# Kernel optimization log

Hardware: AMD Instinct MI355X
Metric: run time of the kernel (lower is better)

Reference implementation:

```python
import jax, jax.numpy as jnp
import numpy as np
from math import sqrt

EMBED = 1024
HEADS = 16

def setup_inputs() -> dict:
    key = jax.random.key(0)
    k1, k2, k3, k4, k5 = jax.random.split(key, 5)
    x = jax.random.normal(k1, (2, 2048, EMBED), dtype=jnp.float32)
    s = 1.0 / sqrt(EMBED)
    W_qkv = jax.random.normal(k2, (EMBED, 3 * EMBED), dtype=jnp.float32) * s
    b_qkv = jax.random.normal(k3, (3 * EMBED,), dtype=jnp.float32) * 0.01
    W_out = jax.random.normal(k4, (EMBED, EMBED), dtype=jnp.float32) * s
    b_out = jax.random.normal(k5, (EMBED,), dtype=jnp.float32) * 0.01
    return {"x": x, "W_qkv": W_qkv, "b_qkv": b_qkv, "W_out": W_out, "b_out": b_out}

def reference(x, W_qkv, b_qkv, W_out, b_out) -> jnp.ndarray:
    B, N, E = x.shape
    H = HEADS
    d = E // H
    qkv = x @ W_qkv + b_qkv                       # [B, N, 3E]
    q, k, v = jnp.split(qkv, 3, axis=2)
    # b n (h e) -> b n h e
    q = q.reshape(B, N, H, d)
    k = k.reshape(B, N, H, d)
    v = v.reshape(B, N, H, d)
    energy = jnp.einsum('bqhe,bkhe->bqhk', q, k)  # [B, N, H, N]
    # NOTE: original divides AFTER softmax, by sqrt(embed_size) (not head dim)
    attn = jax.nn.softmax(energy, axis=-1) / sqrt(E)
    out = jnp.einsum('bihv,bvhd->bihd', attn, v)  # [B, N, H, d]
    out = out.reshape(B, N, E)
    # dropout in eval mode -> identity
    return out @ W_out + b_out
```

## Files before the change

### kernel.cpp

```cpp
#include <hip/hip_runtime.h>
#include <hip/hip_bf16.h>

#define EMBED 1024
#define HEADS 16
#define HDIM 64
#define BATCH 2
#define SEQ 2048
#define ROWS (BATCH*SEQ)
#define QKV_N (3*EMBED)

typedef __attribute__((ext_vector_type(8))) short bf16x8;
typedef __attribute__((ext_vector_type(4))) float f32x4;
typedef __attribute__((ext_vector_type(16))) float f32x16;
typedef __hip_bfloat16 bf16;

__device__ inline f32x4 mfma16(bf16x8 a, bf16x8 b, f32x4 c) {
  return __builtin_amdgcn_mfma_f32_16x16x32_bf16(a, b, c, 0, 0, 0);
}
__device__ inline f32x16 mfma32(bf16x8 a, bf16x8 b, f32x16 c) {
  return __builtin_amdgcn_mfma_f32_32x32x16_bf16(a, b, c, 0, 0, 0);
}
__device__ inline unsigned pk2(float a, float b) {
  union { unsigned u; unsigned short s[2]; } r;
  union { bf16 h; unsigned short v; } ca, cb;
  ca.h = __float2bfloat16(a); cb.h = __float2bfloat16(b);
  r.s[0] = ca.v; r.s[1] = cb.v;
  return r.u;
}

__device__ inline void gload_lds16(const bf16* g, bf16* l) {
  __builtin_amdgcn_global_load_lds(
      (const __attribute__((address_space(1))) unsigned int*)g,
      (__attribute__((address_space(3))) unsigned int*)l, 16, 0, 0);
}

__global__ void cast_x_kernel(const float* __restrict__ in, bf16* __restrict__ out, int n4) {
  int i = blockIdx.x * blockDim.x + threadIdx.x;
  if (i >= n4) return;
  float4 v = reinterpret_cast<const float4*>(in)[i];
  union { ushort4 u; bf16 b[4]; } cv;
  cv.b[0] = __float2bfloat16(v.x);
  cv.b[1] = __float2bfloat16(v.y);
  cv.b[2] = __float2bfloat16(v.z);
  cv.b[3] = __float2bfloat16(v.w);
  reinterpret_cast<ushort4*>(out)[i] = cv.u;
}

__global__ void transpose_cast_kernel(const float* __restrict__ in, bf16* __restrict__ out,
                                      int R, int C) {
  __shared__ float tile[32][33];
  int c0 = blockIdx.x * 32, r0 = blockIdx.y * 32;
  int tx = threadIdx.x, ty = threadIdx.y;
  #pragma unroll
  for (int i = ty; i < 32; i += 8)
    tile[i][tx] = in[(size_t)(r0 + i) * C + c0 + tx];
  __syncthreads();
  #pragma unroll
  for (int i = ty; i < 32; i += 8)
    out[(size_t)(c0 + i) * R + r0 + tx] = __float2bfloat16(tile[tx][i]);
}

__global__ void transpose_v_kernel(const bf16* __restrict__ qkv, bf16* __restrict__ vT) {
  __shared__ bf16 tile[32][33];
  int bh = blockIdx.z, b = bh >> 4, h = bh & 15;
  int t0 = blockIdx.x * 32, d0 = blockIdx.y * 32;
  int tx = threadIdx.x, ty = threadIdx.y;
  #pragma unroll
  for (int i = ty; i < 32; i += 8)
    tile[i][tx] = qkv[(size_t)(b*SEQ + t0 + i) * QKV_N + 2*EMBED + h*HDIM + d0 + tx];
  __syncthreads();
  #pragma unroll
  for (int i = ty; i < 32; i += 8)
    vT[((size_t)bh*HDIM + d0 + i) * SEQ + t0 + tx] = tile[tx][i];
}

template<int OUT_FP32>
__global__ __launch_bounds__(256) void gemm_bias_kernel(
    const bf16* __restrict__ A, const bf16* __restrict__ Bt,
    const float* __restrict__ bias, void* __restrict__ Cout,
    int M, int N, int K) {
  __shared__ __align__(16) bf16 Ash[2][128*32];
  __shared__ __align__(16) bf16 Bsh[2][128*32];
  const int m0 = blockIdx.y * 128, n0 = blockIdx.x * 128;
  const int tid = threadIdx.x, wave = tid >> 6, lane = tid & 63;
  const int wm = wave >> 1, wn = wave & 1;
  const int ll = lane & 15, lg = lane >> 4;
  f32x4 acc[4][4] = {};

  auto STAGE = [&](int t, int buf) {
    const int k0 = t * 32;
    #pragma unroll
    for (int c = 0; c < 2; c++) {
      int li = (wave + c*4) * 64 + lane;
      gload_lds16(A + (size_t)(m0 + (li >> 2)) * K + k0 + (li & 3) * 8,
                  &Ash[buf][(size_t)(wave + c*4) * 512]);
      gload_lds16(Bt + (size_t)(n0 + (li >> 2)) * K + k0 + (li & 3) * 8,
                  &Bsh[buf][(size_t)(wave + c*4) * 512]);
    }
  };

  const int NT = K / 32;
  STAGE(0, 0);
  for (int t = 0; t < NT; t++) {
    const int cur = t & 1;
    if (t < NT - 1) {
      STAGE(t + 1, cur ^ 1);
      asm volatile("s_waitcnt vmcnt(4)" ::: "memory");
    } else {
      asm volatile("s_waitcnt vmcnt(0)" ::: "memory");
    }
    __builtin_amdgcn_s_barrier();
    __builtin_amdgcn_sched_barrier(0);

    bf16x8 af[4], bfr[4];
    #pragma unroll
    for (int mi = 0; mi < 4; mi++)
      af[mi] = *reinterpret_cast<const bf16x8*>(&Ash[cur][(wm*64 + mi*16 + ll)*32 + lg*8]);
    #pragma unroll
    for (int ni = 0; ni < 4; ni++)
      bfr[ni] = *reinterpret_cast<const bf16x8*>(&Bsh[cur][(wn*64 + ni*16 + ll)*32 + lg*8]);
    #pragma unroll
    for (int mi = 0; mi < 4; mi++)
      #pragma unroll
      for (int ni = 0; ni < 4; ni++)
        acc[mi][ni] = mfma16(af[mi], bfr[ni], acc[mi][ni]);

    __builtin_amdgcn_s_barrier();
    __builtin_amdgcn_sched_barrier(0);
  }

  #pragma unroll
  for (int mi = 0; mi < 4; mi++) {
    #pragma unroll
    for (int ni = 0; ni < 4; ni++) {
      int col = n0 + wn*64 + ni*16 + ll;
      float bs = bias[col];
      #pragma unroll
      for (int r = 0; r < 4; r++) {
        int row = m0 + wm*64 + mi*16 + lg*4 + r;
        float v = acc[mi][ni][r] + bs;
        if (OUT_FP32) reinterpret_cast<float*>(Cout)[(size_t)row * N + col] = v;
        else          reinterpret_cast<bf16*>(Cout)[(size_t)row * N + col] = __float2bfloat16(v);
      }
    }
  }
}

__global__ __launch_bounds__(512) void flash_attn11_kernel(
    const bf16* __restrict__ qkv, const bf16* __restrict__ vT, bf16* __restrict__ O) {
  const int lid = blockIdx.y * gridDim.x + blockIdx.x;
  const int wid = (lid & 7) * 64 + (lid >> 3);
  const int qt = wid & 15, bh = wid >> 4;
  const int b = bh >> 4, h = bh & 15;
  const int lane = threadIdx.x & 63, wv = threadIdx.x >> 6;
  const int w_q = wv >> 1, w_s = wv & 1;
  const int q32 = lane & 31, hi = lane >> 5;
  const int qrow = qt * 128 + w_q * 32 + q32;
  const float L2E = 1.44269504088896f;

  __shared__ __align__(16) char smem[65536];
  float* cb_o = (float*)smem;
  float* cb_l = (float*)(smem + 32768);

  const bf16* qp = qkv + (size_t)(b*SEQ + qrow) * QKV_N + h*HDIM + hi*8;
  bf16x8 qf[4];
  #pragma unroll
  for (int ks = 0; ks < 4; ks++)
    qf[ks] = *reinterpret_cast<const bf16x8*>(qp + ks*16);

  float l_run = 0.0f;
  f32x16 oa[2] = {};

  const bf16* kb = qkv + (size_t)(b*SEQ)*QKV_N + EMBED + h*HDIM;
  const bf16* vb = vT + (size_t)bh * HDIM * SEQ;

  const int srow = (lane >> 3);
  const int schunk = (lane & 7) ^ srow;
  const int r0 = w_q * 16;
  const int kt0 = w_s * (SEQ/2);

  auto STAGE = [&](int t, int buf) {
    const int kt = kt0 + t*64;
    bf16* Kd = (bf16*)(smem + buf*32768) + w_s*4096;
    bf16* Vd = (bf16*)(smem + buf*32768 + 16384) + w_s*4096;
    #pragma unroll
    for (int i = 0; i < 2; i++) {
      const int row = r0 + i*8 + srow;
      gload_lds16(kb + (size_t)(kt + row)*QKV_N + schunk*8, Kd + (r0 + i*8)*64);
      gload_lds16(vb + (size_t)row*SEQ + kt + schunk*8,     Vd + (r0 + i*8)*64);
    }
  };

  STAGE(0, 0);
  for (int t = 0; t < 16; t++) {
    const int cur = t & 1;
    if (t < 15) {
      STAGE(t+1, cur^1);
      asm volatile("s_waitcnt vmcnt(4)" ::: "memory");
    } else {
      asm volatile("s_waitcnt vmcnt(0)" ::: "memory");
    }
    __builtin_amdgcn_s_barrier();
    __builtin_amdgcn_sched_barrier(0);

    const bf16* Kl = (const bf16*)(smem + cur*32768) + w_s*4096;
    const bf16* Vl = (const bf16*)(smem + cur*32768 + 16384) + w_s*4096;

    bf16x8 kf[8], vf[8];
    #pragma unroll
    for (int hh = 0; hh < 2; hh++) {
      const int tk = hh*32 + q32;
      #pragma unroll
      for (int ks = 0; ks < 4; ks++)
        kf[hh*4+ks] = *reinterpret_cast<const bf16x8*>(
            Kl + tk*64 + (((ks*2+hi) ^ (tk&7)) << 3));
    }
    #pragma unroll
    for (int dh = 0; dh < 2; dh++) {
      const int dr = dh*32 + q32;
      #pragma unroll
      for (int ks = 0; ks < 4; ks++)
        vf[ks*2+dh] = *reinterpret_cast<const bf16x8*>(
            Vl + dr*64 + (((ks*2+hi) ^ (dr&7)) << 3));
    }

    f32x16 s[2] = {};
    #pragma unroll
    for (int ks = 0; ks < 4; ks++) {
      s[0] = mfma32(kf[ks],   qf[ks], s[0]);
      s[1] = mfma32(kf[4+ks], qf[ks], s[1]);
    }

    float p[32];
    #pragma unroll
    for (int hh = 0; hh < 2; hh++)
      #pragma unroll
      for (int r = 0; r < 16; r++)
        p[hh*16+r] = __builtin_amdgcn_exp2f(s[hh][r] * L2E);

    float a16[16];
    #pragma unroll
    for (int r = 0; r < 16; r++) a16[r] = p[r] + p[r+16];
    #pragma unroll
    for (int r = 0; r < 8; r++) a16[r] += a16[r+8];
    #pragma unroll
    for (int r = 0; r < 4; r++) a16[r] += a16[r+4];
    float rs = (a16[0] + a16[1]) + (a16[2] + a16[3]);
    rs += __shfl_xor(rs, 32);
    l_run += rs;

    union PWU { unsigned w[4]; bf16x8 v; } pw[4];
    #pragma unroll
    for (int hh = 0; hh < 2; hh++) {
      #pragma unroll
      for (int k2 = 0; k2 < 2; k2++) {
        const int b0 = hh*16 + k2*8;
        unsigned WA = pk2(p[b0+0], p[b0+1]);
        unsigned WB = pk2(p[b0+2], p[b0+3]);
        unsigned WC = pk2(p[b0+4], p[b0+5]);
        unsigned WD = pk2(p[b0+6], p[b0+7]);
        asm volatile("v_permlane32_swap_b32 %0, %1" : "+v"(WA), "+v"(WC));
        asm volatile("v_permlane32_swap_b32 %0, %1" : "+v"(WB), "+v"(WD));
        const int ks = hh*2 + k2;
        pw[ks].w[0] = WA;
        pw[ks].w[1] = WB;
        pw[ks].w[2] = WC;
        pw[ks].w[3] = WD;
      }
    }

    #pragma unroll
    for (int ks = 0; ks < 4; ks++) {
      oa[0] = mfma32(vf[ks*2+0], pw[ks].v, oa[0]);
      oa[1] = mfma32(vf[ks*2+1], pw[ks].v, oa[1]);
    }
    __builtin_amdgcn_s_barrier();
    __builtin_amdgcn_sched_barrier(0);
  }

  if (w_s == 1) {
    cb_l[w_q*64 + lane] = l_run;
    #pragma unroll
    for (int dh = 0; dh < 2; dh++)
      #pragma unroll
      for (int r = 0; r < 16; r++)
        cb_o[(w_q*32 + dh*16+r)*64 + lane] = oa[dh][r];
  }
  __syncthreads();
  if (w_s == 0) {
    const float l1 = cb_l[w_q*64 + lane];
    const float inv = 1.0f / ((l_run + l1) * 32.0f);
    bf16* orow = O + (size_t)(b*SEQ + qrow) * EMBED + h*HDIM;
    #pragma unroll
    for (int dh = 0; dh < 2; dh++) {
      #pragma unroll
      for (int tt = 0; tt < 4; tt++) {
        union { ushort4 u; unsigned short s4[4]; } st;
        #pragma unroll
        for (int r = 0; r < 4; r++) {
          float v = (oa[dh][tt*4+r] + cb_o[(w_q*32 + dh*16+tt*4+r)*64 + lane]) * inv;
          union { bf16 hh2; unsigned short v2; } c;
          c.hh2 = __float2bfloat16(v);
          st.s4[r] = c.v2;
        }
        *reinterpret_cast<ushort4*>(orow + dh*32 + tt*8 + hi*4) = st.u;
      }
    }
  }
}

extern "C" void kernel_launch(void* const* d_in, const int* in_sizes, int n_in,
                              void* d_out, int out_size, void* d_ws, size_t ws_size,
                              hipStream_t stream) {
  const float* x     = (const float*)d_in[0];
  const float* W_qkv = (const float*)d_in[1];
  const float* b_qkv = (const float*)d_in[2];
  const float* W_out = (const float*)d_in[3];
  const float* b_out = (const float*)d_in[4];
  float* out = (float*)d_out;

  char* ws = (char*)d_ws;
  bf16* qkv   = (bf16*)(ws);
  bf16* vTb   = (bf16*)(ws + 25165824);
  bf16* Obuf  = (bf16*)(ws + 33554432);
  bf16* xb    = (bf16*)(ws + 41943040);
  bf16* WqkvT = (bf16*)(ws + 50331648);
  bf16* WoutT = (bf16*)(ws + 56623104);

  cast_x_kernel<<<(ROWS*EMBED/4 + 255)/256, 256, 0, stream>>>(x, xb, ROWS*EMBED/4);
  transpose_cast_kernel<<<dim3(QKV_N/32, EMBED/32), dim3(32,8), 0, stream>>>(W_qkv, WqkvT, EMBED, QKV_N);
  transpose_cast_kernel<<<dim3(EMBED/32, EMBED/32), dim3(32,8), 0, stream>>>(W_out, WoutT, EMBED, EMBED);
  gemm_bias_kernel<0><<<dim3(QKV_N/128, ROWS/128), 256, 0, stream>>>(xb, WqkvT, b_qkv, qkv, ROWS, QKV_N, EMBED);
  transpose_v_kernel<<<dim3(SEQ/32, HDIM/32, BATCH*HEADS), dim3(32,8), 0, stream>>>(qkv, vTb);
  flash_attn11_kernel<<<dim3(16, BATCH*HEADS), 512, 0, stream>>>(qkv, vTb, Obuf);
  gemm_bias_kernel<1><<<dim3(EMBED/128, ROWS/128), 256, 0, stream>>>(Obuf, WoutT, b_out, out, ROWS, EMBED, EMBED);
}
```

Baseline: 131.9 us.

## Load V tiles straight to registers and restructure the attention pipeline

V tiles now go straight from global memory into registers, one tile ahead, instead of being staged through LDS. Only K stays double-buffered in shared memory, which halves the LDS footprint. The next K stage is issued after the QK MFMAs, explicit vmcnt waits are placed before the PV MFMAs, and s_setprio is raised around the MFMA blocks. The trailing barrier in the loop is dropped. The aims are less LDS traffic, better overlap of loads with compute, and possibly higher occupancy, at the cost of more VGPRs and uncoalesced 16-byte global V reads that depend on L2 hits.

```diff
diff --git a/kernel.cpp b/kernel.cpp
--- a/kernel.cpp
+++ b/kernel.cpp
@@ -146,7 +146,7 @@
   }
 }
 
-__global__ __launch_bounds__(512) void flash_attn11_kernel(
+__global__ __launch_bounds__(512) void flash_attn12_kernel(
     const bf16* __restrict__ qkv, const bf16* __restrict__ vT, bf16* __restrict__ O) {
   const int lid = blockIdx.y * gridDim.x + blockIdx.x;
   const int wid = (lid & 7) * 64 + (lid >> 3);
@@ -158,7 +158,7 @@
   const int qrow = qt * 128 + w_q * 32 + q32;
   const float L2E = 1.44269504088896f;
 
-  __shared__ __align__(16) char smem[65536];
+  __shared__ __align__(16) char smem[33792];
   float* cb_o = (float*)smem;
   float* cb_l = (float*)(smem + 32768);
 
@@ -179,34 +179,42 @@
   const int r0 = w_q * 16;
   const int kt0 = w_s * (SEQ/2);
 
+  bf16x8 vf[8];
+
   auto STAGE = [&](int t, int buf) {
     const int kt = kt0 + t*64;
-    bf16* Kd = (bf16*)(smem + buf*32768) + w_s*4096;
-    bf16* Vd = (bf16*)(smem + buf*32768 + 16384) + w_s*4096;
+    bf16* Kd = (bf16*)(smem + buf*16384) + w_s*4096;
     #pragma unroll
     for (int i = 0; i < 2; i++) {
       const int row = r0 + i*8 + srow;
       gload_lds16(kb + (size_t)(kt + row)*QKV_N + schunk*8, Kd + (r0 + i*8)*64);
-      gload_lds16(vb + (size_t)row*SEQ + kt + schunk*8,     Vd + (r0 + i*8)*64);
     }
   };
+  auto VLOAD = [&](int t) {
+    const int kt = kt0 + t*64;
+    #pragma unroll
+    for (int dh = 0; dh < 2; dh++) {
+      const int dr = dh*32 + q32;
+      #pragma unroll
+      for (int ks = 0; ks < 4; ks++)
+        vf[ks*2+dh] = *reinterpret_cast<const bf16x8*>(
+            vb + (size_t)dr*SEQ + kt + (ks*2+hi)*8);
+    }
+  };
 
   STAGE(0, 0);
+  asm volatile("" ::: "memory");
+  VLOAD(0);
+
   for (int t = 0; t < 16; t++) {
     const int cur = t & 1;
-    if (t < 15) {
-      STAGE(t+1, cur^1);
-      asm volatile("s_waitcnt vmcnt(4)" ::: "memory");
-    } else {
-      asm volatile("s_waitcnt vmcnt(0)" ::: "memory");
-    }
+    asm volatile("s_waitcnt vmcnt(8)" ::: "memory");
     __builtin_amdgcn_s_barrier();
     __builtin_amdgcn_sched_barrier(0);
 
-    const bf16* Kl = (const bf16*)(smem + cur*32768) + w_s*4096;
-    const bf16* Vl = (const bf16*)(smem + cur*32768 + 16384) + w_s*4096;
-
-    bf16x8 kf[8], vf[8];
+    const bf16* Kl = (const bf16*)(smem + cur*16384) + w_s*4096;
+
+    bf16x8 kf[8];
     #pragma unroll
     for (int hh = 0; hh < 2; hh++) {
       const int tk = hh*32 + q32;
@@ -215,21 +223,18 @@
         kf[hh*4+ks] = *reinterpret_cast<const bf16x8*>(
             Kl + tk*64 + (((ks*2+hi) ^ (tk&7)) << 3));
     }
-    #pragma unroll
-    for (int dh = 0; dh < 2; dh++) {
-      const int dr = dh*32 + q32;
-      #pragma unroll
-      for (int ks = 0; ks < 4; ks++)
-        vf[ks*2+dh] = *reinterpret_cast<const bf16x8*>(
-            Vl + dr*64 + (((ks*2+hi) ^ (dr&7)) << 3));
-    }
 
     f32x16 s[2] = {};
+    __builtin_amdgcn_s_setprio(1);
     #pragma unroll
     for (int ks = 0; ks < 4; ks++) {
       s[0] = mfma32(kf[ks],   qf[ks], s[0]);
       s[1] = mfma32(kf[4+ks], qf[ks], s[1]);
     }
+    __builtin_amdgcn_s_setprio(0);
+
+    if (t < 15) STAGE(t+1, cur^1);
+    __builtin_amdgcn_sched_barrier(0);
 
     float p[32];
     #pragma unroll
@@ -269,15 +274,23 @@
       }
     }
 
+    if (t < 15) { asm volatile("s_waitcnt vmcnt(2)" ::: "memory"); }
+    else        { asm volatile("s_waitcnt vmcnt(0)" ::: "memory"); }
+    __builtin_amdgcn_sched_barrier(0);
+
+    __builtin_amdgcn_s_setprio(1);
     #pragma unroll
     for (int ks = 0; ks < 4; ks++) {
       oa[0] = mfma32(vf[ks*2+0], pw[ks].v, oa[0]);
       oa[1] = mfma32(vf[ks*2+1], pw[ks].v, oa[1]);
     }
-    __builtin_amdgcn_s_barrier();
-    __builtin_amdgcn_sched_barrier(0);
-  }
-
+    __builtin_amdgcn_s_setprio(0);
+
+    if (t < 15) VLOAD(t+1);
+    __builtin_amdgcn_sched_barrier(0);
+  }
+
+  __syncthreads();
   if (w_s == 1) {
     cb_l[w_q*64 + lane] = l_run;
     #pragma unroll
@@ -332,6 +345,6 @@
   transpose_cast_kernel<<<dim3(EMBED/32, EMBED/32), dim3(32,8), 0, stream>>>(W_out, WoutT, EMBED, EMBED);
   gemm_bias_kernel<0><<<dim3(QKV_N/128, ROWS/128), 256, 0, stream>>>(xb, WqkvT, b_qkv, qkv, ROWS, QKV_N, EMBED);
   transpose_v_kernel<<<dim3(SEQ/32, HDIM/32, BATCH*HEADS), dim3(32,8), 0, stream>>>(qkv, vTb);
-  flash_attn11_kernel<<<dim3(16, BATCH*HEADS), 512, 0, stream>>>(qkv, vTb, Obuf);
+  flash_attn12_kernel<<<dim3(16, BATCH*HEADS), 512, 0, stream>>>(qkv, vTb, Obuf);
   gemm_bias_kernel<1><<<dim3(EMBED/128, ROWS/128), 256, 0, stream>>>(Obuf, WoutT, b_out, out, ROWS, EMBED, EMBED);
 }
```

After: 150.6 us. +14.1%, slower.
